# Optimization experiments

Hardware: AMD Instinct MI355X
Metric: run time of the kernel (lower is better)

The kernel has to match this reference:

```python
import jax, jax.numpy as jnp
import numpy as np
from jax import lax

EPS = 1e-5  # torch BatchNorm2d default


def setup_inputs() -> dict:
    key = jax.random.key(0)
    k1, k2, k3 = jax.random.split(key, 3)
    C = 64
    x = jax.random.normal(k1, (32, C, 128, 128), dtype=jnp.float32)
    # per-channel 3x3 depthwise weights (OIHW with I=1, feature_group_count=C)
    w = jax.random.normal(k2, (C, 1, 3, 3), dtype=jnp.float32) * (1.0 / 3.0)
    b = jax.random.normal(k3, (C,), dtype=jnp.float32) * 0.1
    gamma = jnp.ones((C,), dtype=jnp.float32)
    beta = jnp.zeros((C,), dtype=jnp.float32)
    return {"x": x, "w": w, "b": b, "gamma": gamma, "beta": beta}


def reference(x, w, b, gamma, beta):
    C = x.shape[1]
    # depthwise 3x3 conv, stride 1, padding 1 (same math as C separate Conv2d(1,1,3))
    y = lax.conv_general_dilated(
        x, w,
        window_strides=(1, 1),
        padding=((1, 1), (1, 1)),
        feature_group_count=C,
        dimension_numbers=("NCHW", "OIHW", "NCHW"),
    )
    y = y + b[None, :, None, None]
    # BatchNorm2d(1) per channel in training mode: batch stats over (N, H, W),
    # biased variance, eps=1e-5
    mean = jnp.mean(y, axis=(0, 2, 3), keepdims=True)
    var = jnp.var(y, axis=(0, 2, 3), keepdims=True)
    y_hat = (y - mean) * lax.rsqrt(var + EPS)
    out = y_hat * gamma[None, :, None, None] + beta[None, :, None, None]
    return jax.nn.relu(out)
```

## Files before the change

kernel.cpp:

```cpp
#include <hip/hip_runtime.h>

#define HW        128
#define PLANE     16384
#define NCH       64
#define NB        32
#define NQ        4
#define NPART     8192
#define COUNT_INV (1.0f / 524288.0f)
#define EPSV      1e-5f

#define YELEMS    (NB * NCH * PLANE)
#define PART_OFF  (YELEMS / 2)
#define WS_NEED   ((size_t)YELEMS * 2 + 16384 * 4)

typedef float    f4v __attribute__((ext_vector_type(4)));
typedef _Float16 h4v __attribute__((ext_vector_type(4)));


__device__ __forceinline__ void load_win(const float* __restrict__ bp, int r0, int w4,
                                         bool hasL, bool hasR, float (&v)[6][6]) {
#pragma unroll
    for (int i = 0; i < 6; ++i) {
        int g = r0 - 1 + i;
        if ((unsigned)g < (unsigned)HW) {
            const float* rp = bp + g * HW + w4;
            float4 m = *(const float4*)rp;
            v[i][0] = hasL ? rp[-1] : 0.f;
            v[i][1] = m.x; v[i][2] = m.y; v[i][3] = m.z; v[i][4] = m.w;
            v[i][5] = hasR ? rp[4] : 0.f;
        } else {
#pragma unroll
            for (int j = 0; j < 6; ++j) v[i][j] = 0.f;
        }
    }
}

__device__ __forceinline__ void conv_row(const float (&tp)[6], const float (&md)[6],
                                         const float (&bt)[6], const float* W,
                                         float bias, float (&acc)[4]) {
#pragma unroll
    for (int j = 0; j < 4; ++j) {
        float a = bias;
        a = fmaf(tp[j],     W[0], a);
        a = fmaf(tp[j + 1], W[1], a);
        a = fmaf(tp[j + 2], W[2], a);
        a = fmaf(md[j],     W[3], a);
        a = fmaf(md[j + 1], W[4], a);
        a = fmaf(md[j + 2], W[5], a);
        a = fmaf(bt[j],     W[6], a);
        a = fmaf(bt[j + 1], W[7], a);
        a = fmaf(bt[j + 2], W[8], a);
        acc[j] = a;
    }
}

__global__ __launch_bounds__(256) void pass_conv_stats(const float* __restrict__ x,
                                                       const float* __restrict__ wgt,
                                                       const float* __restrict__ bias,
                                                       _Float16* __restrict__ yh,
                                                       float* __restrict__ partials) {
    __shared__ float red[8];
    const int bid   = blockIdx.x;
    const int q     = bid & 3;
    const int plane = bid >> 2;
    const int c     = plane & 63;
    const int n     = plane >> 6;
    const int t     = threadIdx.x;
    const int cg    = t & 31, rg = t >> 5;
    const int w4    = cg * 4, r0 = q * 32 + rg * 4;
    const bool hasL = (cg != 0), hasR = (cg != 31);

    float W[9];
#pragma unroll
    for (int k = 0; k < 9; ++k) W[k] = wgt[c * 9 + k];
    const float bv = bias[c];
    const float* bp = x + (size_t)plane * PLANE;
    _Float16* yp = yh + (size_t)plane * PLANE;

    float v[6][6];
    load_win(bp, r0, w4, hasL, hasR, v);

    float sum = 0.f, sq = 0.f;
#pragma unroll
    for (int k = 0; k < 4; ++k) {
        float acc[4];
        conv_row(v[k], v[k + 1], v[k + 2], W, bv, acc);
        h4v hv;
        hv.x = (_Float16)acc[0]; hv.y = (_Float16)acc[1];
        hv.z = (_Float16)acc[2]; hv.w = (_Float16)acc[3];
        *(h4v*)(yp + (r0 + k) * HW + w4) = hv;
#pragma unroll
        for (int j = 0; j < 4; ++j) {
            sum += acc[j];
            sq = fmaf(acc[j], acc[j], sq);
        }
    }

#pragma unroll
    for (int off = 32; off; off >>= 1) {
        sum += __shfl_down(sum, off);
        sq  += __shfl_down(sq, off);
    }
    const int wave = t >> 6, lane = t & 63;
    if (lane == 0) { red[wave] = sum; red[4 + wave] = sq; }
    __syncthreads();
    if (t == 0) {
        const int pi = n * 4 + q;
        partials[c * 128 + pi]         = red[0] + red[1] + red[2] + red[3];
        partials[NPART + c * 128 + pi] = red[4] + red[5] + red[6] + red[7];
    }
}

__global__ __launch_bounds__(256) void pass_norm(const _Float16* __restrict__ yh,
                                                 const float* __restrict__ partials,
                                                 const float* __restrict__ gamma,
                                                 const float* __restrict__ beta,
                                                 float* __restrict__ out) {
    const int bid   = blockIdx.x;
    const int q     = bid & 3;
    const int plane = bid >> 2;
    const int c     = plane & 63;
    const int t     = threadIdx.x;
    const int cg    = t & 31, rg = t >> 5;
    const int w4    = cg * 4, r0 = q * 32 + rg * 4;

    const _Float16* yp = yh + (size_t)plane * PLANE;

    h4v hv[4];
#pragma unroll
    for (int k = 0; k < 4; ++k)
        hv[k] = *(const h4v*)(yp + (r0 + k) * HW + w4);

    const int lane = t & 63;
    float S = partials[c * 128 + lane]         + partials[c * 128 + 64 + lane];
    float Q = partials[NPART + c * 128 + lane] + partials[NPART + c * 128 + 64 + lane];
#pragma unroll
    for (int off = 32; off; off >>= 1) {
        S += __shfl_xor(S, off);
        Q += __shfl_xor(Q, off);
    }
    const float mean = S * COUNT_INV;
    const float var  = fmaxf(Q * COUNT_INV - mean * mean, 0.f);
    const float s    = gamma[c] * rsqrtf(var + EPSV);
    const float sh   = beta[c] - mean * s;

    float* op = out + (size_t)plane * PLANE;
#pragma unroll
    for (int k = 0; k < 4; ++k) {
        f4v o;
        o.x = fmaxf(fmaf((float)hv[k].x, s, sh), 0.f);
        o.y = fmaxf(fmaf((float)hv[k].y, s, sh), 0.f);
        o.z = fmaxf(fmaf((float)hv[k].z, s, sh), 0.f);
        o.w = fmaxf(fmaf((float)hv[k].w, s, sh), 0.f);
        __builtin_nontemporal_store(o, (f4v*)(op + (r0 + k) * HW + w4));
    }
}

__global__ __launch_bounds__(256) void pass_stats_fb(const float* __restrict__ x,
                                                     const float* __restrict__ wgt,
                                                     const float* __restrict__ bias,
                                                     float* __restrict__ partials) {
    __shared__ float red[8];
    const int bid   = blockIdx.x;
    const int q     = bid & 3;
    const int plane = bid >> 2;
    const int c     = plane & 63;
    const int n     = plane >> 6;
    const int t     = threadIdx.x;
    const int cg    = t & 31, rg = t >> 5;
    const int w4    = cg * 4, r0 = q * 32 + rg * 4;
    const bool hasL = (cg != 0), hasR = (cg != 31);

    float W[9];
#pragma unroll
    for (int k = 0; k < 9; ++k) W[k] = wgt[c * 9 + k];
    const float bv = bias[c];
    const float* bp = x + (size_t)plane * PLANE;

    float v[6][6];
    load_win(bp, r0, w4, hasL, hasR, v);

    float sum = 0.f, sq = 0.f;
#pragma unroll
    for (int k = 0; k < 4; ++k) {
        float acc[4];
        conv_row(v[k], v[k + 1], v[k + 2], W, bv, acc);
#pragma unroll
        for (int j = 0; j < 4; ++j) { sum += acc[j]; sq = fmaf(acc[j], acc[j], sq); }
    }
#pragma unroll
    for (int off = 32; off; off >>= 1) {
        sum += __shfl_down(sum, off);
        sq  += __shfl_down(sq, off);
    }
    const int wave = t >> 6, lane = t & 63;
    if (lane == 0) { red[wave] = sum; red[4 + wave] = sq; }
    __syncthreads();
    if (t == 0) {
        const int pi = n * 4 + q;
        partials[c * 128 + pi]         = red[0] + red[1] + red[2] + red[3];
        partials[NPART + c * 128 + pi] = red[4] + red[5] + red[6] + red[7];
    }
}

__global__ __launch_bounds__(256) void pass_apply_fb(const float* __restrict__ x,
                                                     const float* __restrict__ wgt,
                                                     const float* __restrict__ bias,
                                                     const float* __restrict__ partials,
                                                     const float* __restrict__ gamma,
                                                     const float* __restrict__ beta,
                                                     float* __restrict__ out) {
    const int bid   = blockIdx.x;
    const int q     = bid & 3;
    const int plane = bid >> 2;
    const int c     = plane & 63;
    const int t     = threadIdx.x;
    const int cg    = t & 31, rg = t >> 5;
    const int w4    = cg * 4, r0 = q * 32 + rg * 4;
    const bool hasL = (cg != 0), hasR = (cg != 31);

    float W[9];
#pragma unroll
    for (int k = 0; k < 9; ++k) W[k] = wgt[c * 9 + k];
    const float bv = bias[c];
    const float* bp = x + (size_t)plane * PLANE;

    float v[6][6];
    load_win(bp, r0, w4, hasL, hasR, v);

    const int lane = t & 63;
    float S = partials[c * 128 + lane]         + partials[c * 128 + 64 + lane];
    float Q = partials[NPART + c * 128 + lane] + partials[NPART + c * 128 + 64 + lane];
#pragma unroll
    for (int off = 32; off; off >>= 1) {
        S += __shfl_xor(S, off);
        Q += __shfl_xor(Q, off);
    }
    const float mean = S * COUNT_INV;
    const float var  = fmaxf(Q * COUNT_INV - mean * mean, 0.f);
    const float s    = gamma[c] * rsqrtf(var + EPSV);
    const float sh   = fmaf(bv, s, beta[c] - mean * s);

    float* op = out + (size_t)plane * PLANE;
#pragma unroll
    for (int k = 0; k < 4; ++k) {
        float acc[4];
        conv_row(v[k], v[k + 1], v[k + 2], W, 0.f, acc);
        f4v o;
        o.x = fmaxf(fmaf(acc[0], s, sh), 0.f);
        o.y = fmaxf(fmaf(acc[1], s, sh), 0.f);
        o.z = fmaxf(fmaf(acc[2], s, sh), 0.f);
        o.w = fmaxf(fmaf(acc[3], s, sh), 0.f);
        __builtin_nontemporal_store(o, (f4v*)(op + (r0 + k) * HW + w4));
    }
}

extern "C" void kernel_launch(void* const* d_in, const int* in_sizes, int n_in,
                              void* d_out, int out_size, void* d_ws, size_t ws_size,
                              hipStream_t stream) {
    const float* x     = (const float*)d_in[0];
    const float* w     = (const float*)d_in[1];
    const float* b     = (const float*)d_in[2];
    const float* gamma = (const float*)d_in[3];
    const float* beta  = (const float*)d_in[4];
    float* out = (float*)d_out;

    if (ws_size >= WS_NEED) {
        _Float16* yh  = (_Float16*)d_ws;
        float* parts  = (float*)d_ws + PART_OFF;
        pass_conv_stats<<<NB * NCH * NQ, 256, 0, stream>>>(x, w, b, yh, parts);
        pass_norm<<<NB * NCH * NQ, 256, 0, stream>>>(yh, parts, gamma, beta, out);
    } else {
        float* parts = (float*)d_ws;
        pass_stats_fb<<<NB * NCH * NQ, 256, 0, stream>>>(x, w, b, parts);
        pass_apply_fb<<<NB * NCH * NQ, 256, 0, stream>>>(x, w, b, parts, gamma, beta, out);
    }
}
```

Before: 73.04 us.

## Fuse conv, stats and normalize into one cooperative kernel with register-held outputs

Replaces the two-pass conv+stats / normalize scheme with a single cooperative kernel of 1024 blocks. Each block computes two full planes of one channel, keeps the fp16 conv results in registers, writes per-plane partial sums, does a grid-wide sync, then normalizes from registers and writes the output. This drops the fp16 intermediate round trip through global memory and one kernel launch. In exchange it adds a grid barrier, a per-call occupancy query on the host, high register pressure (64 packed half2 per thread), and removes the no-workspace fallback path.

```diff
diff --git a/kernel.cpp b/kernel.cpp
--- a/kernel.cpp
+++ b/kernel.cpp
@@ -1,4 +1,7 @@
 #include <hip/hip_runtime.h>
+#include <hip/hip_cooperative_groups.h>
+
+namespace cg = cooperative_groups;
 
 #define HW        128
 #define PLANE     16384
@@ -14,8 +17,8 @@
 #define WS_NEED   ((size_t)YELEMS * 2 + 16384 * 4)
 
 typedef float    f4v __attribute__((ext_vector_type(4)));
+typedef _Float16 h2v __attribute__((ext_vector_type(2)));
 typedef _Float16 h4v __attribute__((ext_vector_type(4)));
-
 
 __device__ __forceinline__ void load_win(const float* __restrict__ bp, int r0, int w4,
                                          bool hasL, bool hasR, float (&v)[6][6]) {
@@ -51,6 +54,122 @@
         a = fmaf(bt[j + 1], W[7], a);
         a = fmaf(bt[j + 2], W[8], a);
         acc[j] = a;
+    }
+}
+
+__global__ __launch_bounds__(256, 4) void fused(const float* __restrict__ x,
+                                                const float* __restrict__ wgt,
+                                                const float* __restrict__ bias,
+                                                const float* __restrict__ gamma,
+                                                const float* __restrict__ beta,
+                                                float* __restrict__ partials,
+                                                float* __restrict__ out) {
+    __shared__ float red[8];
+    __shared__ float ssh[2];
+    const int bid = blockIdx.x;
+    const int c   = bid & 63;
+    const int np  = bid >> 6;
+    const int t   = threadIdx.x;
+    const int cg_ = t & 31, rg = t >> 5;
+    const int w4  = cg_ * 4;
+    const bool hasL = (cg_ != 0), hasR = (cg_ != 31);
+
+    float W[9];
+#pragma unroll
+    for (int k = 0; k < 9; ++k) W[k] = wgt[c * 9 + k];
+    const float bv = bias[c];
+
+    h2v yr0[32];
+    h2v yr1[32];
+
+#pragma unroll
+    for (int pp = 0; pp < 2; ++pp) {
+        const int n = np * 2 + pp;
+        const int plane = n * NCH + c;
+        const float* bp = x + (size_t)plane * PLANE;
+        h2v* yr = pp ? yr1 : yr0;
+
+        float sum = 0.f, sq = 0.f;
+#pragma unroll
+        for (int k = 0; k < 4; ++k) {
+            const int r0 = rg * 16 + k * 4;
+            float v[6][6];
+            load_win(bp, r0, w4, hasL, hasR, v);
+#pragma unroll
+            for (int rr = 0; rr < 4; ++rr) {
+                float acc[4];
+                conv_row(v[rr], v[rr + 1], v[rr + 2], W, bv, acc);
+                h2v a, b;
+                a.x = (_Float16)acc[0]; a.y = (_Float16)acc[1];
+                b.x = (_Float16)acc[2]; b.y = (_Float16)acc[3];
+                yr[k * 8 + rr * 2]     = a;
+                yr[k * 8 + rr * 2 + 1] = b;
+#pragma unroll
+                for (int j = 0; j < 4; ++j) {
+                    sum += acc[j];
+                    sq = fmaf(acc[j], acc[j], sq);
+                }
+            }
+        }
+#pragma unroll
+        for (int off = 32; off; off >>= 1) {
+            sum += __shfl_down(sum, off);
+            sq  += __shfl_down(sq, off);
+        }
+        const int wave = t >> 6, lane = t & 63;
+        if (lane == 0) { red[wave] = sum; red[4 + wave] = sq; }
+        __syncthreads();
+        if (t == 0) {
+            partials[c * 32 + n]        = red[0] + red[1] + red[2] + red[3];
+            partials[2048 + c * 32 + n] = red[4] + red[5] + red[6] + red[7];
+        }
+        __syncthreads();
+    }
+
+    __threadfence();
+    cg::this_grid().sync();
+
+    if (t < 32) {
+        float S = partials[c * 32 + t];
+        float Q = partials[2048 + c * 32 + t];
+#pragma unroll
+        for (int off = 16; off; off >>= 1) {
+            S += __shfl_xor(S, off);
+            Q += __shfl_xor(Q, off);
+        }
+        if (t == 0) {
+            float mean = S * COUNT_INV;
+            float var  = fmaxf(Q * COUNT_INV - mean * mean, 0.f);
+            float s    = gamma[c] * rsqrtf(var + EPSV);
+            ssh[0] = s;
+            ssh[1] = beta[c] - mean * s;
+        }
+    }
+    __syncthreads();
+    const float s  = ssh[0];
+    const float sh = ssh[1];
+
+#pragma unroll
+    for (int pp = 0; pp < 2; ++pp) {
+        const int n = np * 2 + pp;
+        const int plane = n * NCH + c;
+        float* op = out + (size_t)plane * PLANE;
+        h2v* yr = pp ? yr1 : yr0;
+#pragma unroll
+        for (int k = 0; k < 4; ++k) {
+#pragma unroll
+            for (int rr = 0; rr < 4; ++rr) {
+                h2v a = yr[k * 8 + rr * 2];
+                h2v b = yr[k * 8 + rr * 2 + 1];
+                f4v o;
+                o.x = fmaxf(fmaf((float)a.x, s, sh), 0.f);
+                o.y = fmaxf(fmaf((float)a.y, s, sh), 0.f);
+                o.z = fmaxf(fmaf((float)b.x, s, sh), 0.f);
+                o.w = fmaxf(fmaf((float)b.y, s, sh), 0.f);
+                const int row = rg * 16 + k * 4 + rr;
+                __builtin_nontemporal_store(o, (f4v*)(op + row * HW + w4));
+            }
+        }
     }
 }
 
@@ -90,12 +209,8 @@
         hv.z = (_Float16)acc[2]; hv.w = (_Float16)acc[3];
         *(h4v*)(yp + (r0 + k) * HW + w4) = hv;
 #pragma unroll
-        for (int j = 0; j < 4; ++j) {
-            sum += acc[j];
-            sq = fmaf(acc[j], acc[j], sq);
-        }
-    }
-
+        for (int j = 0; j < 4; ++j) { sum += acc[j]; sq = fmaf(acc[j], acc[j], sq); }
+    }
 #pragma unroll
     for (int off = 32; off; off >>= 1) {
         sum += __shfl_down(sum, off);
@@ -125,7 +240,6 @@
     const int w4    = cg * 4, r0 = q * 32 + rg * 4;
 
     const _Float16* yp = yh + (size_t)plane * PLANE;
-
     h4v hv[4];
 #pragma unroll
     for (int k = 0; k < 4; ++k)
@@ -152,105 +266,6 @@
         o.y = fmaxf(fmaf((float)hv[k].y, s, sh), 0.f);
         o.z = fmaxf(fmaf((float)hv[k].z, s, sh), 0.f);
         o.w = fmaxf(fmaf((float)hv[k].w, s, sh), 0.f);
-        __builtin_nontemporal_store(o, (f4v*)(op + (r0 + k) * HW + w4));
-    }
-}
-
-__global__ __launch_bounds__(256) void pass_stats_fb(const float* __restrict__ x,
-                                                     const float* __restrict__ wgt,
-                                                     const float* __restrict__ bias,
-                                                     float* __restrict__ partials) {
-    __shared__ float red[8];
-    const int bid   = blockIdx.x;
-    const int q     = bid & 3;
-    const int plane = bid >> 2;
-    const int c     = plane & 63;
-    const int n     = plane >> 6;
-    const int t     = threadIdx.x;
-    const int cg    = t & 31, rg = t >> 5;
-    const int w4    = cg * 4, r0 = q * 32 + rg * 4;
-    const bool hasL = (cg != 0), hasR = (cg != 31);
-
-    float W[9];
-#pragma unroll
-    for (int k = 0; k < 9; ++k) W[k] = wgt[c * 9 + k];
-    const float bv = bias[c];
-    const float* bp = x + (size_t)plane * PLANE;
-
-    float v[6][6];
-    load_win(bp, r0, w4, hasL, hasR, v);
-
-    float sum = 0.f, sq = 0.f;
-#pragma unroll
-    for (int k = 0; k < 4; ++k) {
-        float acc[4];
-        conv_row(v[k], v[k + 1], v[k + 2], W, bv, acc);
-#pragma unroll
-        for (int j = 0; j < 4; ++j) { sum += acc[j]; sq = fmaf(acc[j], acc[j], sq); }
-    }
-#pragma unroll
-    for (int off = 32; off; off >>= 1) {
-        sum += __shfl_down(sum, off);
-        sq  += __shfl_down(sq, off);
-    }
-    const int wave = t >> 6, lane = t & 63;
-    if (lane == 0) { red[wave] = sum; red[4 + wave] = sq; }
-    __syncthreads();
-    if (t == 0) {
-        const int pi = n * 4 + q;
-        partials[c * 128 + pi]         = red[0] + red[1] + red[2] + red[3];
-        partials[NPART + c * 128 + pi] = red[4] + red[5] + red[6] + red[7];
-    }
-}
-
-__global__ __launch_bounds__(256) void pass_apply_fb(const float* __restrict__ x,
-                                                     const float* __restrict__ wgt,
-                                                     const float* __restrict__ bias,
-                                                     const float* __restrict__ partials,
-                                                     const float* __restrict__ gamma,
-                                                     const float* __restrict__ beta,
-                                                     float* __restrict__ out) {
-    const int bid   = blockIdx.x;
-    const int q     = bid & 3;
-    const int plane = bid >> 2;
-    const int c     = plane & 63;
-    const int t     = threadIdx.x;
-    const int cg    = t & 31, rg = t >> 5;
-    const int w4    = cg * 4, r0 = q * 32 + rg * 4;
-    const bool hasL = (cg != 0), hasR = (cg != 31);
-
-    float W[9];
-#pragma unroll
-    for (int k = 0; k < 9; ++k) W[k] = wgt[c * 9 + k];
-    const float bv = bias[c];
-    const float* bp = x + (size_t)plane * PLANE;
-
-    float v[6][6];
-    load_win(bp, r0, w4, hasL, hasR, v);
-
-    const int lane = t & 63;
-    float S = partials[c * 128 + lane]         + partials[c * 128 + 64 + lane];
-    float Q = partials[NPART + c * 128 + lane] + partials[NPART + c * 128 + 64 + lane];
-#pragma unroll
-    for (int off = 32; off; off >>= 1) {
-        S += __shfl_xor(S, off);
-        Q += __shfl_xor(Q, off);
-    }
-    const float mean = S * COUNT_INV;
-    const float var  = fmaxf(Q * COUNT_INV - mean * mean, 0.f);
-    const float s    = gamma[c] * rsqrtf(var + EPSV);
-    const float sh   = fmaf(bv, s, beta[c] - mean * s);
-
-    float* op = out + (size_t)plane * PLANE;
-#pragma unroll
-    for (int k = 0; k < 4; ++k) {
-        float acc[4];
-        conv_row(v[k], v[k + 1], v[k + 2], W, 0.f, acc);
-        f4v o;
-        o.x = fmaxf(fmaf(acc[0], s, sh), 0.f);
-        o.y = fmaxf(fmaf(acc[1], s, sh), 0.f);
-        o.z = fmaxf(fmaf(acc[2], s, sh), 0.f);
-        o.w = fmaxf(fmaf(acc[3], s, sh), 0.f);
         __builtin_nontemporal_store(o, (f4v*)(op + (r0 + k) * HW + w4));
     }
 }
@@ -265,14 +280,22 @@
     const float* beta  = (const float*)d_in[4];
     float* out = (float*)d_out;
 
-    if (ws_size >= WS_NEED) {
+    int nb = 0;
+    hipError_t qe = hipOccupancyMaxActiveBlocksPerMultiprocessor(
+        &nb, reinterpret_cast<const void*>(fused), 256, 0);
+
+    if (qe == hipSuccess && nb >= 4) {
+        float* parts = (float*)d_ws;
+        const float* xa = x; const float* wa = w; const float* ba = b;
+        const float* ga = gamma; const float* be = beta;
+        float* pw = parts; float* oa = out;
+        void* args[] = {&xa, &wa, &ba, &ga, &be, &pw, &oa};
+        hipLaunchCooperativeKernel(reinterpret_cast<const void*>(fused),
+                                   dim3(1024), dim3(256), args, 0, stream);
+    } else if (ws_size >= WS_NEED) {
         _Float16* yh  = (_Float16*)d_ws;
         float* parts  = (float*)d_ws + PART_OFF;
         pass_conv_stats<<<NB * NCH * NQ, 256, 0, stream>>>(x, w, b, yh, parts);
         pass_norm<<<NB * NCH * NQ, 256, 0, stream>>>(yh, parts, gamma, beta, out);
-    } else {
-        float* parts = (float*)d_ws;
-        pass_stats_fb<<<NB * NCH * NQ, 256, 0, stream>>>(x, w, b, parts);
-        pass_apply_fb<<<NB * NCH * NQ, 256, 0, stream>>>(x, w, b, parts, gamma, beta, out);
-    }
-}
+    }
+}
```

Measured after the change: 73.03 us. About the same (-0.0%).
